# Optimization experiments

Hardware: AMD Instinct MI355X
Metric: run time of the kernel (lower is better)

Reference implementation:

```python
import jax, jax.numpy as jnp
import numpy as np

B, S, D, H = 4, 2048, 768, 12
DH = D // H  # 64


def setup_inputs() -> dict:
    key = jax.random.key(0)
    ks = jax.random.split(key, 7)
    return {
        "sequences": jax.random.normal(ks[0], (B, S, D), dtype=jnp.float32),
        "wq": jax.random.normal(ks[1], (H, DH, DH), dtype=jnp.float32) / np.sqrt(DH),
        "bq": jax.random.normal(ks[2], (H, DH), dtype=jnp.float32) * 0.02,
        "wk": jax.random.normal(ks[3], (H, DH, DH), dtype=jnp.float32) / np.sqrt(DH),
        "bk": jax.random.normal(ks[4], (H, DH), dtype=jnp.float32) * 0.02,
        "wv": jax.random.normal(ks[5], (H, DH, DH), dtype=jnp.float32) / np.sqrt(DH),
        "bv": jax.random.normal(ks[6], (H, DH), dtype=jnp.float32) * 0.02,
    }


def reference(sequences, wq, bq, wk, bk, wv, bv):
    # split channels into heads: [B, S, H, DH]
    xh = sequences.reshape(B, S, H, DH)
    # per-head linear projections (weight applied as x @ W^T + b, matching nn.Linear)
    q = jnp.einsum("bshd,hed->bshe", xh, wq) + bq  # [B,S,H,DH]
    k = jnp.einsum("bshd,hed->bshe", xh, wk) + bk
    v = jnp.einsum("bshd,hed->bshe", xh, wv) + bv
    scale = 1.0 / np.sqrt(DH).astype(np.float32)
    scores = jnp.einsum("bqhd,bkhd->bhqk", q, k) * scale  # [B,H,S,S]
    attn = jax.nn.softmax(scores, axis=-1)
    out = jnp.einsum("bhqk,bkhd->bqhd", attn, v)  # [B,S,H,DH]
    return out.reshape(B, S, D)
```

## Files before the change

kernel.cpp:

```cpp
#include <hip/hip_runtime.h>

#define NB 4
#define NS 2048
#define ND 768
#define NH 12
#define NDH 64
#define XPITCH 72
#define SSCALE 0.18033688011112043f

typedef __bf16 bf16x8 __attribute__((ext_vector_type(8)));
typedef float  f32x4  __attribute__((ext_vector_type(4)));
typedef unsigned int u32;

#define MFMA16(a, b, c) __builtin_amdgcn_mfma_f32_16x16x32_bf16(a, b, c, 0, 0, 0)

__device__ __forceinline__ u32 packbf(float a, float b) {
    u32 ua = __builtin_bit_cast(u32, a) + 0x8000u;
    u32 ub = __builtin_bit_cast(u32, b) + 0x8000u;
    return __builtin_amdgcn_perm(ub, ua, 0x07060302u);
}

__device__ __forceinline__ bf16x8 cvt8(float4 a, float4 b) {
    union { u32 u[4]; bf16x8 v; } r;
    r.u[0] = packbf(a.x, a.y); r.u[1] = packbf(a.z, a.w);
    r.u[2] = packbf(b.x, b.y); r.u[3] = packbf(b.z, b.w);
    return r.v;
}

__device__ __forceinline__ __bf16 f2bf(float f) {
    u32 u = __builtin_bit_cast(u32, f) + 0x8000u;
    unsigned short s = (unsigned short)(u >> 16);
    return __builtin_bit_cast(__bf16, s);
}

__device__ __forceinline__ void gld16(const __bf16* g, __bf16* l) {
    __builtin_amdgcn_global_load_lds(
        (const __attribute__((address_space(1))) u32*)g,
        (__attribute__((address_space(3))) u32*)l, 16, 0, 0);
}

__global__ __launch_bounds__(256, 2) void proj_kernel(
    const float* __restrict__ x,
    const float* __restrict__ wq, const float* __restrict__ bq,
    const float* __restrict__ wk, const float* __restrict__ bk,
    const float* __restrict__ wv, const float* __restrict__ bv,
    __bf16* __restrict__ qws, __bf16* __restrict__ kws, __bf16* __restrict__ vtws)
{
    const int st = blockIdx.x, h = blockIdx.y, b = blockIdx.z;
    const int sbase = st * 128;
    const int tid = threadIdx.x;

    __shared__ __align__(16) __bf16 Xs[64 * XPITCH];
    __shared__ __align__(16) __bf16 Tv[64 * XPITCH];

    const int r = tid >> 2, f = tid & 3;
    const int lane = tid & 63, w = tid >> 6, col = lane & 15, quad = lane >> 4;

    const size_t wrow = (size_t)(h * NDH + w * 16 + col) * NDH;
    const float* wq0 = wq + wrow + quad * 8;
    const float* wk0 = wk + wrow + quad * 8;
    const float* wv0 = wv + wrow + quad * 8;
    const bf16x8 wqa0 = cvt8(*(const float4*)(wq0),      *(const float4*)(wq0 + 4));
    const bf16x8 wqa1 = cvt8(*(const float4*)(wq0 + 32), *(const float4*)(wq0 + 36));
    const bf16x8 wka0 = cvt8(*(const float4*)(wk0),      *(const float4*)(wk0 + 4));
    const bf16x8 wka1 = cvt8(*(const float4*)(wk0 + 32), *(const float4*)(wk0 + 36));
    const bf16x8 wva0 = cvt8(*(const float4*)(wv0),      *(const float4*)(wv0 + 4));
    const bf16x8 wva1 = cvt8(*(const float4*)(wv0 + 32), *(const float4*)(wv0 + 36));

    float bqs[4], bks[4], bvs[4];
#pragma unroll
    for (int rr = 0; rr < 4; ++rr) {
        const int e = h * NDH + w * 16 + quad * 4 + rr;
        bqs[rr] = bq[e] * SSCALE;
        bks[rr] = bk[e];
        bvs[rr] = bv[e];
    }

    const size_t bh = (size_t)(b * NH + h);

    float4 xr[4];
    {
        const float* xrow = x + (size_t)(b * NS + sbase + r) * ND + h * NDH + f * 16;
        xr[0] = *(const float4*)(xrow);
        xr[1] = *(const float4*)(xrow + 4);
        xr[2] = *(const float4*)(xrow + 8);
        xr[3] = *(const float4*)(xrow + 12);
    }

    for (int sub = 0; sub < 2; ++sub) {
        const int s0 = sbase + sub * 64;

        *(bf16x8*)&Xs[r * XPITCH + f * 16]     = cvt8(xr[0], xr[1]);
        *(bf16x8*)&Xs[r * XPITCH + f * 16 + 8] = cvt8(xr[2], xr[3]);
        __syncthreads();

        if (sub == 0) {
            const float* xrow = x + (size_t)(b * NS + sbase + 64 + r) * ND + h * NDH + f * 16;
            xr[0] = *(const float4*)(xrow);
            xr[1] = *(const float4*)(xrow + 4);
            xr[2] = *(const float4*)(xrow + 8);
            xr[3] = *(const float4*)(xrow + 12);
        }

        bf16x8 xb0[4], xb1[4];
#pragma unroll
        for (int nt = 0; nt < 4; ++nt) {
            xb0[nt] = *(const bf16x8*)&Xs[(nt * 16 + col) * XPITCH + quad * 8];
            xb1[nt] = *(const bf16x8*)&Xs[(nt * 16 + col) * XPITCH + 32 + quad * 8];
        }

#pragma unroll
        for (int nt = 0; nt < 4; ++nt) {
            f32x4 aq = {0.f, 0.f, 0.f, 0.f};
            f32x4 ak = {0.f, 0.f, 0.f, 0.f};
            f32x4 av = {0.f, 0.f, 0.f, 0.f};
            aq = MFMA16(wqa0, xb0[nt], aq); aq = MFMA16(wqa1, xb1[nt], aq);
            ak = MFMA16(wka0, xb0[nt], ak); ak = MFMA16(wka1, xb1[nt], ak);
            av = MFMA16(wva0, xb0[nt], av); av = MFMA16(wva1, xb1[nt], av);

            union { u32 u[2]; uint2 v; } pq, pk;
            pq.u[0] = packbf(fmaf(aq[0], SSCALE, bqs[0]), fmaf(aq[1], SSCALE, bqs[1]));
            pq.u[1] = packbf(fmaf(aq[2], SSCALE, bqs[2]), fmaf(aq[3], SSCALE, bqs[3]));
            pk.u[0] = packbf(ak[0] + bks[0], ak[1] + bks[1]);
            pk.u[1] = packbf(ak[2] + bks[2], ak[3] + bks[3]);
            const size_t goff = (bh * NS + s0 + nt * 16 + col) * NDH + w * 16 + quad * 4;
            *(uint2*)(qws + goff) = pq.v;
            *(uint2*)(kws + goff) = pk.v;

            const int pos = ((nt >> 1) << 5) + ((col >> 2) << 3) + ((nt & 1) << 2) + (col & 3);
#pragma unroll
            for (int rr = 0; rr < 4; ++rr)
                Tv[(w * 16 + quad * 4 + rr) * XPITCH + pos] = f2bf(av[rr] + bvs[rr]);
        }
        __syncthreads();

        {
            const uint4 v0 = *(const uint4*)&Tv[r * XPITCH + f * 16];
            const uint4 v1 = *(const uint4*)&Tv[r * XPITCH + f * 16 + 8];
            __bf16* vdst = vtws + (bh * NDH + r) * NS + s0 + f * 16;
            *(uint4*)vdst = v0; *(uint4*)(vdst + 8) = v1;
        }
        __syncthreads();
    }
}

__global__ __launch_bounds__(256, 2) void attn_kernel(
    const __bf16* __restrict__ qws, const __bf16* __restrict__ kws,
    const __bf16* __restrict__ vtws, float* __restrict__ out)
{
    const int qt = blockIdx.x, h = blockIdx.y, b = blockIdx.z;
    const int q0 = qt * 64;
    const int tid = threadIdx.x;

    __shared__ __align__(16) unsigned char smem[65536];
    __bf16* lds = (__bf16*)smem;
    float* slabA = (float*)smem;
    float* slabB = (float*)(smem + 17408);
    float* mbuf  = (float*)(smem + 34816);
    float* lbuf  = mbuf + 256;

    const size_t bh = (size_t)(b * NH + h);
    const int lane = tid & 63, w = tid >> 6, col = lane & 15, quad = lane >> 4;

    bf16x8 qb0[4], qb1[4];
#pragma unroll
    for (int nt = 0; nt < 4; ++nt) {
        const __bf16* qp = qws + (bh * NS + q0 + nt * 16 + col) * NDH + quad * 8;
        qb0[nt] = *(const bf16x8*)(qp);
        qb1[nt] = *(const bf16x8*)(qp + 32);
    }

    const int rK = tid >> 3;
    const int qdK = (tid & 7) ^ (rK & 7);
    const __bf16* ksrc = kws + bh * (size_t)NS * NDH + rK * NDH + qdK * 8;
    const int rV = tid >> 4;
    const int qdV = (tid & 15) ^ (rV & 7);
    const __bf16* vsrc = vtws + (bh * (size_t)NDH + rV) * NS + qdV * 8;

    const int cx7 = col & 7;
    int ka_off[2][2], va_off[4];
#pragma unroll
    for (int mt = 0; mt < 2; ++mt) {
        const int rr = w * 32 + mt * 16 + col;
        ka_off[mt][0] = rr * 64 + ((quad)     ^ cx7) * 8;
        ka_off[mt][1] = rr * 64 + ((quad + 4) ^ cx7) * 8;
    }
#pragma unroll
    for (int dt = 0; dt < 4; ++dt) {
        const int rr = dt * 16 + col;
        va_off[dt] = 8192 + rr * 128 + ((w * 4 + quad) ^ cx7) * 8;
    }

    float m[4], l[4];
#pragma unroll
    for (int nt = 0; nt < 4; ++nt) { m[nt] = -__builtin_inff(); l[nt] = 0.f; }
    f32x4 o[4][4];
#pragma unroll
    for (int dt = 0; dt < 4; ++dt)
#pragma unroll
        for (int nt = 0; nt < 4; ++nt) o[dt][nt] = (f32x4){0.f, 0.f, 0.f, 0.f};

    {
        __bf16* kdst = lds + tid * 8;
        __bf16* vdst = lds + 8192 + tid * 8;
#pragma unroll
        for (int i = 0; i < 4; ++i) gld16(ksrc + i * 2048, kdst + i * 2048);
#pragma unroll
        for (int i = 0; i < 4; ++i) gld16(vsrc + i * 32768, vdst + i * 2048);
    }
    __syncthreads();

    for (int kt = 0; kt < NS / 128; ++kt) {
        const int cur = (kt & 1) * 16384;
        if (kt + 1 < NS / 128) {
            const int nxt = ((kt + 1) & 1) * 16384;
            __bf16* kdst = lds + nxt + tid * 8;
            __bf16* vdst = lds + nxt + 8192 + tid * 8;
            const __bf16* ks = ksrc + (size_t)(kt + 1) * 8192;
            const __bf16* vs = vsrc + (kt + 1) * 128;
#pragma unroll
            for (int i = 0; i < 4; ++i) gld16(ks + i * 2048, kdst + i * 2048);
#pragma unroll
            for (int i = 0; i < 4; ++i) gld16(vs + i * 32768, vdst + i * 2048);
        }

        bf16x8 ka[2][2], va[4];
#pragma unroll
        for (int mt = 0; mt < 2; ++mt) {
            ka[mt][0] = *(const bf16x8*)&lds[cur + ka_off[mt][0]];
            ka[mt][1] = *(const bf16x8*)&lds[cur + ka_off[mt][1]];
        }
#pragma unroll
        for (int dt = 0; dt < 4; ++dt) va[dt] = *(const bf16x8*)&lds[cur + va_off[dt]];

#pragma unroll
        for (int nt = 0; nt < 4; ++nt) {
            f32x4 sA = {0.f, 0.f, 0.f, 0.f};
            f32x4 sB = {0.f, 0.f, 0.f, 0.f};
            sA = MFMA16(ka[0][0], qb0[nt], sA); sA = MFMA16(ka[0][1], qb1[nt], sA);
            sB = MFMA16(ka[1][0], qb0[nt], sB); sB = MFMA16(ka[1][1], qb1[nt], sB);

            float rowm = fmaxf(fmaxf(fmaxf(sA[0], sA[1]), fmaxf(sA[2], sA[3])),
                               fmaxf(fmaxf(sB[0], sB[1]), fmaxf(sB[2], sB[3])));
            rowm = fmaxf(rowm, __shfl_xor(rowm, 16, 64));
            rowm = fmaxf(rowm, __shfl_xor(rowm, 32, 64));

            const float mn = fmaxf(m[nt], rowm);
            const float al = __builtin_amdgcn_exp2f(m[nt] - mn);
            m[nt] = mn;

            const float p0 = __builtin_amdgcn_exp2f(sA[0] - mn);
            const float p1 = __builtin_amdgcn_exp2f(sA[1] - mn);
            const float p2 = __builtin_amdgcn_exp2f(sA[2] - mn);
            const float p3 = __builtin_amdgcn_exp2f(sA[3] - mn);
            const float p4 = __builtin_amdgcn_exp2f(sB[0] - mn);
            const float p5 = __builtin_amdgcn_exp2f(sB[1] - mn);
            const float p6 = __builtin_amdgcn_exp2f(sB[2] - mn);
            const float p7 = __builtin_amdgcn_exp2f(sB[3] - mn);
            float rs = ((p0 + p1) + (p2 + p3)) + ((p4 + p5) + (p6 + p7));
            rs += __shfl_xor(rs, 16, 64);
            rs += __shfl_xor(rs, 32, 64);
            l[nt] = l[nt] * al + rs;

            union { u32 u[4]; bf16x8 v; } pb;
            pb.u[0] = packbf(p0, p1);
            pb.u[1] = packbf(p2, p3);
            pb.u[2] = packbf(p4, p5);
            pb.u[3] = packbf(p6, p7);

#pragma unroll
            for (int dt = 0; dt < 4; ++dt) {
                o[dt][nt] *= al;
                o[dt][nt] = MFMA16(va[dt], pb.v, o[dt][nt]);
            }
        }
        __syncthreads();
    }

    if (quad == 0) {
#pragma unroll
        for (int nt = 0; nt < 4; ++nt) {
            mbuf[w * 64 + nt * 16 + col] = m[nt];
            lbuf[w * 64 + nt * 16 + col] = l[nt];
        }
    }
    __syncthreads();

    float scale[4];
#pragma unroll
    for (int nt = 0; nt < 4; ++nt) {
        const int qi = nt * 16 + col;
        const float m0 = mbuf[qi], m1 = mbuf[64 + qi], m2 = mbuf[128 + qi], m3 = mbuf[192 + qi];
        const float M = fmaxf(fmaxf(m0, m1), fmaxf(m2, m3));
        const float L = lbuf[qi]       * __builtin_amdgcn_exp2f(m0 - M)
                      + lbuf[64 + qi]  * __builtin_amdgcn_exp2f(m1 - M)
                      + lbuf[128 + qi] * __builtin_amdgcn_exp2f(m2 - M)
                      + lbuf[192 + qi] * __builtin_amdgcn_exp2f(m3 - M);
        scale[nt] = __builtin_amdgcn_exp2f(m[nt] - M) / L;
    }
    __syncthreads();
#pragma unroll
    for (int dt = 0; dt < 4; ++dt)
#pragma unroll
        for (int nt = 0; nt < 4; ++nt) o[dt][nt] *= scale[nt];

    if (w == 0 || w == 2) {
        float* s = (w == 0) ? slabA : slabB;
#pragma unroll
        for (int dt = 0; dt < 4; ++dt)
#pragma unroll
            for (int nt = 0; nt < 4; ++nt)
                *(f32x4*)&s[(nt * 16 + col) * 68 + dt * 16 + quad * 4] = o[dt][nt];
    }
    __syncthreads();
    if (w == 1 || w == 3) {
        float* s = (w == 1) ? slabA : slabB;
#pragma unroll
        for (int dt = 0; dt < 4; ++dt)
#pragma unroll
            for (int nt = 0; nt < 4; ++nt) {
                f32x4* p = (f32x4*)&s[(nt * 16 + col) * 68 + dt * 16 + quad * 4];
                *p = *p + o[dt][nt];
            }
    }
    __syncthreads();

    const int qr = tid >> 2, fq = tid & 3;
#pragma unroll
    for (int j = 0; j < 4; ++j) {
        const f32x4 a = *(const f32x4*)&slabA[qr * 68 + fq * 16 + j * 4];
        const f32x4 c = *(const f32x4*)&slabB[qr * 68 + fq * 16 + j * 4];
        *(f32x4*)&out[(size_t)(b * NS + q0 + qr) * ND + h * NDH + fq * 16 + j * 4] = a + c;
    }
}

extern "C" void kernel_launch(void* const* d_in, const int* in_sizes, int n_in,
                              void* d_out, int out_size, void* d_ws, size_t ws_size,
                              hipStream_t stream) {
    (void)in_sizes; (void)n_in; (void)out_size; (void)ws_size;
    const float* x  = (const float*)d_in[0];
    const float* wq = (const float*)d_in[1];
    const float* bq = (const float*)d_in[2];
    const float* wk = (const float*)d_in[3];
    const float* bk = (const float*)d_in[4];
    const float* wv = (const float*)d_in[5];
    const float* bv = (const float*)d_in[6];
    float* out = (float*)d_out;

    __bf16* qws  = (__bf16*)d_ws;
    __bf16* kws  = qws + (size_t)NB * NH * NS * NDH;
    __bf16* vtws = kws + (size_t)NB * NH * NS * NDH;

    dim3 pgrid(NS / 128, NH, NB);
    proj_kernel<<<pgrid, 256, 0, stream>>>(x, wq, bq, wk, bk, wv, bv, qws, kws, vtws);
    dim3 agrid(NS / 64, NH, NB);
    attn_kernel<<<agrid, 256, 0, stream>>>(qws, kws, vtws, out);
}
```

Before: 195.5 us.

## Make attention K/V tiles wave-private, stage Q in LDS, skip rescale

In the attention kernel, each wave now loads its own slice of K and V into a single wave-private LDS region. Explicit vmcnt/lgkmcnt waits replace the double-buffered shared tiles and the per-iteration __syncthreads, which cuts LDS to 40 KB so occupancy can rise to 4 blocks per CU. Q is staged in LDS instead of held in registers, and the online-softmax rescale of o and l is skipped when no row max increases (checked with a ballot). The projection kernel now transposes Q and K through LDS so they are written with coalesced 16-byte stores. The risks are exposed load latency, since one buffer is overwritten after the waits, and extra LDS reads for Q.

New measurement: 221.9 us. 13.5% more time.

```diff
diff --git a/kernel.cpp b/kernel.cpp
--- a/kernel.cpp
+++ b/kernel.cpp
@@ -5,6 +5,7 @@
 #define ND 768
 #define NH 12
 #define NDH 64
+#define NT (NS / 128)
 #define XPITCH 72
 #define SSCALE 0.18033688011112043f
 
@@ -13,6 +14,10 @@
 typedef unsigned int u32;
 
 #define MFMA16(a, b, c) __builtin_amdgcn_mfma_f32_16x16x32_bf16(a, b, c, 0, 0, 0)
+
+#define WAITVM4()  asm volatile("s_waitcnt vmcnt(4)" ::: "memory")
+#define WAITVM0()  asm volatile("s_waitcnt vmcnt(0)" ::: "memory")
+#define WAITLGKM() asm volatile("s_waitcnt lgkmcnt(0)" ::: "memory")
 
 __device__ __forceinline__ u32 packbf(float a, float b) {
     u32 ua = __builtin_bit_cast(u32, a) + 0x8000u;
@@ -39,7 +44,7 @@
         (__attribute__((address_space(3))) u32*)l, 16, 0, 0);
 }
 
-__global__ __launch_bounds__(256, 2) void proj_kernel(
+__global__ __launch_bounds__(256, 4) void proj_kernel(
     const float* __restrict__ x,
     const float* __restrict__ wq, const float* __restrict__ bq,
     const float* __restrict__ wk, const float* __restrict__ bk,
@@ -51,6 +56,8 @@
     const int tid = threadIdx.x;
 
     __shared__ __align__(16) __bf16 Xs[64 * XPITCH];
+    __shared__ __align__(16) __bf16 Tq[64 * XPITCH];
+    __shared__ __align__(16) __bf16 Tk[64 * XPITCH];
     __shared__ __align__(16) __bf16 Tv[64 * XPITCH];
 
     const int r = tid >> 2, f = tid & 3;
@@ -102,30 +109,25 @@
             xr[3] = *(const float4*)(xrow + 12);
         }
 
-        bf16x8 xb0[4], xb1[4];
 #pragma unroll
         for (int nt = 0; nt < 4; ++nt) {
-            xb0[nt] = *(const bf16x8*)&Xs[(nt * 16 + col) * XPITCH + quad * 8];
-            xb1[nt] = *(const bf16x8*)&Xs[(nt * 16 + col) * XPITCH + 32 + quad * 8];
-        }
-
-#pragma unroll
-        for (int nt = 0; nt < 4; ++nt) {
+            const bf16x8 xb0 = *(const bf16x8*)&Xs[(nt * 16 + col) * XPITCH + quad * 8];
+            const bf16x8 xb1 = *(const bf16x8*)&Xs[(nt * 16 + col) * XPITCH + 32 + quad * 8];
             f32x4 aq = {0.f, 0.f, 0.f, 0.f};
             f32x4 ak = {0.f, 0.f, 0.f, 0.f};
             f32x4 av = {0.f, 0.f, 0.f, 0.f};
-            aq = MFMA16(wqa0, xb0[nt], aq); aq = MFMA16(wqa1, xb1[nt], aq);
-            ak = MFMA16(wka0, xb0[nt], ak); ak = MFMA16(wka1, xb1[nt], ak);
-            av = MFMA16(wva0, xb0[nt], av); av = MFMA16(wva1, xb1[nt], av);
+            aq = MFMA16(wqa0, xb0, aq); aq = MFMA16(wqa1, xb1, aq);
+            ak = MFMA16(wka0, xb0, ak); ak = MFMA16(wka1, xb1, ak);
+            av = MFMA16(wva0, xb0, av); av = MFMA16(wva1, xb1, av);
 
             union { u32 u[2]; uint2 v; } pq, pk;
             pq.u[0] = packbf(fmaf(aq[0], SSCALE, bqs[0]), fmaf(aq[1], SSCALE, bqs[1]));
             pq.u[1] = packbf(fmaf(aq[2], SSCALE, bqs[2]), fmaf(aq[3], SSCALE, bqs[3]));
             pk.u[0] = packbf(ak[0] + bks[0], ak[1] + bks[1]);
             pk.u[1] = packbf(ak[2] + bks[2], ak[3] + bks[3]);
-            const size_t goff = (bh * NS + s0 + nt * 16 + col) * NDH + w * 16 + quad * 4;
-            *(uint2*)(qws + goff) = pq.v;
-            *(uint2*)(kws + goff) = pk.v;
+            const int soff = (nt * 16 + col) * XPITCH + w * 16 + quad * 4;
+            *(uint2*)&Tq[soff] = pq.v;
+            *(uint2*)&Tk[soff] = pk.v;
 
             const int pos = ((nt >> 1) << 5) + ((col >> 2) << 3) + ((nt & 1) << 2) + (col & 3);
 #pragma unroll
@@ -135,6 +137,16 @@
         __syncthreads();
 
         {
+            const uint4 a0 = *(const uint4*)&Tq[r * XPITCH + f * 16];
+            const uint4 a1 = *(const uint4*)&Tq[r * XPITCH + f * 16 + 8];
+            __bf16* qdst = qws + (bh * NS + s0 + r) * NDH + f * 16;
+            *(uint4*)qdst = a0; *(uint4*)(qdst + 8) = a1;
+
+            const uint4 k0 = *(const uint4*)&Tk[r * XPITCH + f * 16];
+            const uint4 k1 = *(const uint4*)&Tk[r * XPITCH + f * 16 + 8];
+            __bf16* kdst = kws + (bh * NS + s0 + r) * NDH + f * 16;
+            *(uint4*)kdst = k0; *(uint4*)(kdst + 8) = k1;
+
             const uint4 v0 = *(const uint4*)&Tv[r * XPITCH + f * 16];
             const uint4 v1 = *(const uint4*)&Tv[r * XPITCH + f * 16 + 8];
             __bf16* vdst = vtws + (bh * NDH + r) * NS + s0 + f * 16;
@@ -144,7 +156,7 @@
     }
 }
 
-__global__ __launch_bounds__(256, 2) void attn_kernel(
+__global__ __launch_bounds__(256, 4) void attn_kernel(
     const __bf16* __restrict__ qws, const __bf16* __restrict__ kws,
     const __bf16* __restrict__ vtws, float* __restrict__ out)
 {
@@ -152,7 +164,7 @@
     const int q0 = qt * 64;
     const int tid = threadIdx.x;
 
-    __shared__ __align__(16) unsigned char smem[65536];
+    __shared__ __align__(16) unsigned char smem[40960];
     __bf16* lds = (__bf16*)smem;
     float* slabA = (float*)smem;
     float* slabB = (float*)(smem + 17408);
@@ -161,34 +173,31 @@
 
     const size_t bh = (size_t)(b * NH + h);
     const int lane = tid & 63, w = tid >> 6, col = lane & 15, quad = lane >> 4;
-
-    bf16x8 qb0[4], qb1[4];
+    const int L = lane;
+
+    const __bf16* ksrc = kws + bh * (size_t)(NS * NDH)
+                       + (size_t)(w * 32 + (L >> 3)) * NDH + ((L & 7) ^ (L >> 3)) * 8;
+    const __bf16* vsrc = vtws + bh * (size_t)(NDH * NS)
+                       + (size_t)(L >> 2) * NS + w * 32 + ((L & 3) ^ ((L >> 3) & 3)) * 8;
+    __bf16* kdst0 = lds + w * 2048 + L * 8;
+    __bf16* vdst0 = lds + 8192 + w * 2048 + L * 8;
+
+    const int cx7 = col & 7;
+    int ka_off[2][2], va_off[4], qoff0[4], qoff1[4];
+#pragma unroll
+    for (int mt = 0; mt < 2; ++mt) {
+        const int base = w * 2048 + (mt * 16 + col) * 64;
+        ka_off[mt][0] = base + ((quad)     ^ cx7) * 8;
+        ka_off[mt][1] = base + ((quad + 4) ^ cx7) * 8;
+    }
+#pragma unroll
+    for (int dt = 0; dt < 4; ++dt)
+        va_off[dt] = 8192 + w * 2048 + (dt * 16 + col) * 32 + (quad ^ ((col >> 1) & 3)) * 8;
 #pragma unroll
     for (int nt = 0; nt < 4; ++nt) {
-        const __bf16* qp = qws + (bh * NS + q0 + nt * 16 + col) * NDH + quad * 8;
-        qb0[nt] = *(const bf16x8*)(qp);
-        qb1[nt] = *(const bf16x8*)(qp + 32);
-    }
-
-    const int rK = tid >> 3;
-    const int qdK = (tid & 7) ^ (rK & 7);
-    const __bf16* ksrc = kws + bh * (size_t)NS * NDH + rK * NDH + qdK * 8;
-    const int rV = tid >> 4;
-    const int qdV = (tid & 15) ^ (rV & 7);
-    const __bf16* vsrc = vtws + (bh * (size_t)NDH + rV) * NS + qdV * 8;
-
-    const int cx7 = col & 7;
-    int ka_off[2][2], va_off[4];
-#pragma unroll
-    for (int mt = 0; mt < 2; ++mt) {
-        const int rr = w * 32 + mt * 16 + col;
-        ka_off[mt][0] = rr * 64 + ((quad)     ^ cx7) * 8;
-        ka_off[mt][1] = rr * 64 + ((quad + 4) ^ cx7) * 8;
-    }
-#pragma unroll
-    for (int dt = 0; dt < 4; ++dt) {
-        const int rr = dt * 16 + col;
-        va_off[dt] = 8192 + rr * 128 + ((w * 4 + quad) ^ cx7) * 8;
+        const int base = 16384 + (nt * 16 + col) * 64;
+        qoff0[nt] = base + ((quad)     ^ cx7) * 8;
+        qoff1[nt] = base + ((quad + 4) ^ cx7) * 8;
     }
 
     float m[4], l[4];
@@ -201,53 +210,66 @@
         for (int nt = 0; nt < 4; ++nt) o[dt][nt] = (f32x4){0.f, 0.f, 0.f, 0.f};
 
     {
-        __bf16* kdst = lds + tid * 8;
-        __bf16* vdst = lds + 8192 + tid * 8;
-#pragma unroll
-        for (int i = 0; i < 4; ++i) gld16(ksrc + i * 2048, kdst + i * 2048);
-#pragma unroll
-        for (int i = 0; i < 4; ++i) gld16(vsrc + i * 32768, vdst + i * 2048);
-    }
-    __syncthreads();
-
-    for (int kt = 0; kt < NS / 128; ++kt) {
-        const int cur = (kt & 1) * 16384;
-        if (kt + 1 < NS / 128) {
-            const int nxt = ((kt + 1) & 1) * 16384;
-            __bf16* kdst = lds + nxt + tid * 8;
-            __bf16* vdst = lds + nxt + 8192 + tid * 8;
+        const int row = tid >> 3;
+        const int d = (tid & 7) ^ (row & 7);
+        const __bf16* qs = qws + (bh * NS + q0 + row) * (size_t)NDH + d * 8;
+        __bf16* qdst = lds + 16384 + tid * 8;
+        gld16(qs, qdst);
+        gld16(qs + 32 * NDH, qdst + 2048);
+    }
+#pragma unroll
+    for (int i = 0; i < 4; ++i) gld16(ksrc + i * 512, kdst0 + i * 512);
+#pragma unroll
+    for (int i = 0; i < 4; ++i) gld16(vsrc + (size_t)i * 16 * NS, vdst0 + i * 512);
+    __syncthreads();
+
+    for (int kt = 0; kt < NT; ++kt) {
+        WAITVM4();
+        bf16x8 ka[2][2];
+#pragma unroll
+        for (int mt = 0; mt < 2; ++mt) {
+            ka[mt][0] = *(const bf16x8*)&lds[ka_off[mt][0]];
+            ka[mt][1] = *(const bf16x8*)&lds[ka_off[mt][1]];
+        }
+        WAITVM0();
+        bf16x8 va[4];
+#pragma unroll
+        for (int dt = 0; dt < 4; ++dt) va[dt] = *(const bf16x8*)&lds[va_off[dt]];
+        WAITLGKM();
+
+        if (kt + 1 < NT) {
             const __bf16* ks = ksrc + (size_t)(kt + 1) * 8192;
             const __bf16* vs = vsrc + (kt + 1) * 128;
 #pragma unroll
-            for (int i = 0; i < 4; ++i) gld16(ks + i * 2048, kdst + i * 2048);
-#pragma unroll
-            for (int i = 0; i < 4; ++i) gld16(vs + i * 32768, vdst + i * 2048);
-        }
-
-        bf16x8 ka[2][2], va[4];
-#pragma unroll
-        for (int mt = 0; mt < 2; ++mt) {
-            ka[mt][0] = *(const bf16x8*)&lds[cur + ka_off[mt][0]];
-            ka[mt][1] = *(const bf16x8*)&lds[cur + ka_off[mt][1]];
-        }
-#pragma unroll
-        for (int dt = 0; dt < 4; ++dt) va[dt] = *(const bf16x8*)&lds[cur + va_off[dt]];
+            for (int i = 0; i < 4; ++i) gld16(ks + i * 512, kdst0 + i * 512);
+#pragma unroll
+            for (int i = 0; i < 4; ++i) gld16(vs + (size_t)i * 16 * NS, vdst0 + i * 512);
+        }
 
 #pragma unroll
         for (int nt = 0; nt < 4; ++nt) {
+            const bf16x8 qb0 = *(const bf16x8*)&lds[qoff0[nt]];
+            const bf16x8 qb1 = *(const bf16x8*)&lds[qoff1[nt]];
             f32x4 sA = {0.f, 0.f, 0.f, 0.f};
             f32x4 sB = {0.f, 0.f, 0.f, 0.f};
-            sA = MFMA16(ka[0][0], qb0[nt], sA); sA = MFMA16(ka[0][1], qb1[nt], sA);
-            sB = MFMA16(ka[1][0], qb0[nt], sB); sB = MFMA16(ka[1][1], qb1[nt], sB);
+            sA = MFMA16(ka[0][0], qb0, sA); sA = MFMA16(ka[0][1], qb1, sA);
+            sB = MFMA16(ka[1][0], qb0, sB); sB = MFMA16(ka[1][1], qb1, sB);
 
             float rowm = fmaxf(fmaxf(fmaxf(sA[0], sA[1]), fmaxf(sA[2], sA[3])),
                                fmaxf(fmaxf(sB[0], sB[1]), fmaxf(sB[2], sB[3])));
             rowm = fmaxf(rowm, __shfl_xor(rowm, 16, 64));
             rowm = fmaxf(rowm, __shfl_xor(rowm, 32, 64));
 
-            const float mn = fmaxf(m[nt], rowm);
-            const float al = __builtin_amdgcn_exp2f(m[nt] - mn);
-            m[nt] = mn;
+            const float mo = m[nt];
+            float mn = mo;
+            if (__ballot(rowm > mo) != 0ULL) {
+                mn = fmaxf(mo, rowm);
+                const float al = __builtin_amdgcn_exp2f(mo - mn);
+                m[nt] = mn;
+                l[nt] *= al;
+#pragma unroll
+                for (int dt = 0; dt < 4; ++dt) o[dt][nt] *= al;
+            }
 
             const float p0 = __builtin_amdgcn_exp2f(sA[0] - mn);
             const float p1 = __builtin_amdgcn_exp2f(sA[1] - mn);
@@ -260,7 +282,7 @@
             float rs = ((p0 + p1) + (p2 + p3)) + ((p4 + p5) + (p6 + p7));
             rs += __shfl_xor(rs, 16, 64);
             rs += __shfl_xor(rs, 32, 64);
-            l[nt] = l[nt] * al + rs;
+            l[nt] += rs;
 
             union { u32 u[4]; bf16x8 v; } pb;
             pb.u[0] = packbf(p0, p1);
@@ -269,14 +291,12 @@
             pb.u[3] = packbf(p6, p7);
 
 #pragma unroll
-            for (int dt = 0; dt < 4; ++dt) {
-                o[dt][nt] *= al;
+            for (int dt = 0; dt < 4; ++dt)
                 o[dt][nt] = MFMA16(va[dt], pb.v, o[dt][nt]);
-            }
-        }
-        __syncthreads();
-    }
-
+        }
+    }
+
+    __syncthreads();
     if (quad == 0) {
 #pragma unroll
         for (int nt = 0; nt < 4; ++nt) {
@@ -292,11 +312,11 @@
         const int qi = nt * 16 + col;
         const float m0 = mbuf[qi], m1 = mbuf[64 + qi], m2 = mbuf[128 + qi], m3 = mbuf[192 + qi];
         const float M = fmaxf(fmaxf(m0, m1), fmaxf(m2, m3));
-        const float L = lbuf[qi]       * __builtin_amdgcn_exp2f(m0 - M)
-                      + lbuf[64 + qi]  * __builtin_amdgcn_exp2f(m1 - M)
-                      + lbuf[128 + qi] * __builtin_amdgcn_exp2f(m2 - M)
-                      + lbuf[192 + qi] * __builtin_amdgcn_exp2f(m3 - M);
-        scale[nt] = __builtin_amdgcn_exp2f(m[nt] - M) / L;
+        const float Lt = lbuf[qi]       * __builtin_amdgcn_exp2f(m0 - M)
+                       + lbuf[64 + qi]  * __builtin_amdgcn_exp2f(m1 - M)
+                       + lbuf[128 + qi] * __builtin_amdgcn_exp2f(m2 - M)
+                       + lbuf[192 + qi] * __builtin_amdgcn_exp2f(m3 - M);
+        scale[nt] = __builtin_amdgcn_exp2f(m[nt] - M) / Lt;
     }
     __syncthreads();
 #pragma unroll
```
